# Kernel optimization log

Hardware: AMD Instinct MI355X
Metric: run time of the kernel (lower is better)

## Reference

```python
import jax, jax.numpy as jnp
import numpy as np

B, S, D, H, E, K, DH = 4, 1024, 1024, 8, 4, 2, 128


def setup_inputs() -> dict:
    key = jax.random.key(0)
    ks = jax.random.split(key, 9)
    std = 1.0 / np.sqrt(D)
    f = lambda k, shape, s: jax.random.normal(k, shape, dtype=jnp.float32) * s
    return {
        'q_src': f(ks[0], (B, S, D), 1.0),
        'k_src': f(ks[1], (B, S, D), 1.0),
        'v_src': f(ks[2], (B, S, D), 1.0),
        'Wq': f(ks[3], (H * DH, D), std),
        'Wk': f(ks[4], (H * DH, D), std),
        'Wv': f(ks[5], (H * E, D, DH), std),
        'Wo': f(ks[6], (H * E, DH, D), 1.0 / np.sqrt(H * DH)),
        'sel_v': f(ks[7], (H * E, D), std),
        'sel_o': f(ks[8], (H * E, D), std),
    }


def _route(src, selw):
    # sigmoid-gated per-head top-k expert selection (get_sel), eval mode
    g = jax.nn.sigmoid((src @ selw.T).reshape(*src.shape[:-1], H, E))  # [B,S,H,E]
    val, idx = jax.lax.top_k(g, K)
    # dense per-expert mixture weights: zeros except top-k sigmoid gates
    return (jax.nn.one_hot(idx, E, dtype=g.dtype) * val[..., None]).sum(-2)  # [B,S,H,E]


def reference(q_src, k_src, v_src, Wq, Wk, Wv, Wo, sel_v, sel_o):
    scale = (1.0 / np.sqrt(DH)) ** 0.5  # scale.sqrt() applied to both q and k
    q = ((q_src @ Wq.T) * scale).reshape(B, S, H, DH).transpose(0, 2, 1, 3)  # [B,H,S,DH]
    k = ((k_src @ Wk.T) * scale).reshape(B, S, H, DH).transpose(0, 2, 1, 3)

    wv = _route(k_src, sel_v)  # [B,S,H,E] V-expert gates (from keys)
    wo = _route(q_src, sel_o)  # [B,S,H,E] O-expert gates (from queries)

    # cvmm V: per-token top-k mixture of expert V projections
    v_all = jnp.einsum('bsd,hedc->bshec', v_src, Wv.reshape(H, E, D, DH))
    v = jnp.einsum('bshec,bshe->bhsc', v_all, wv)  # [B,H,S,DH]

    att = jax.nn.softmax(jnp.einsum('bhqc,bhkc->bhqk', q, k), axis=-1)
    res = jnp.einsum('bhqk,bhkc->bqhc', att, v)  # [B,S,H,DH]

    # cvmm O: weight per-head outputs by gates, project and sum over heads/experts
    resw = res[..., None, :] * wo[..., None]  # [B,S,H,E,DH]
    out = jnp.einsum('bshec,hecd->bsd', resw, Wo.reshape(H, E, DH, D))
    return out
```

## Files before the change

### kernel.cpp

```cpp
#include <hip/hip_runtime.h>

#define DEV __device__ __forceinline__

typedef __attribute__((ext_vector_type(8))) short s8v;
typedef __attribute__((ext_vector_type(4))) short s4v;
typedef __attribute__((ext_vector_type(4))) float f4v;

DEV unsigned short f2b(float f){
    unsigned u = __float_as_uint(f);
    u = (u + 0x7FFFu + ((u >> 16) & 1u)) >> 16;
    return (unsigned short)u;
}
DEV float b2f(short s){ return __uint_as_float(((unsigned)(unsigned short)s) << 16); }

DEV unsigned cvtpk(float lo, float hi){
    unsigned r;
    asm("v_cvt_pk_bf16_f32 %0, %1, %2" : "=v"(r) : "v"(lo), "v"(hi));
    return r;
}
DEV float exp2v(float x){
    float r;
    asm("v_exp_f32 %0, %1" : "=v"(r) : "v"(x));
    return r;
}

DEV void gload16(const void* g, void* l){
    __builtin_amdgcn_global_load_lds(
        (const __attribute__((address_space(1))) unsigned*)g,
        (__attribute__((address_space(3))) unsigned*)l, 16, 0, 0);
}


DEV void stage2(const short* A, const short* B, int sA, int sB, int kA, int kB,
                short* la, short* lb, int w, int lane){
    int srow = lane >> 3;
    int swcol = ((lane & 7) ^ srow) << 3;
    #pragma unroll
    for(int it = 0; it < 4; it++){
        int seg = (w << 2) + it;
        int row = (seg << 3) + srow;
        gload16(&A[(size_t)row * sA + kA + swcol], &la[seg << 9]);
        gload16(&B[(size_t)row * sB + kB + swcol], &lb[seg << 9]);
    }
}

DEV void mfma_block(const short* la, const short* lb, int wm, int wn, int qr, int grp, f4v acc[4][4]){
    #pragma unroll
    for(int ks = 0; ks < 2; ks++){
        s8v af[4], bf[4];
        #pragma unroll
        for(int m = 0; m < 4; m++)
            af[m] = *(const s8v*)&la[(wm + m * 16 + qr) * 64 + ((((ks << 2) + grp) ^ (qr & 7)) << 3)];
        #pragma unroll
        for(int n = 0; n < 4; n++)
            bf[n] = *(const s8v*)&lb[(wn + n * 16 + qr) * 64 + ((((ks << 2) + grp) ^ (qr & 7)) << 3)];
        #pragma unroll
        for(int m = 0; m < 4; m++)
            #pragma unroll
            for(int n = 0; n < 4; n++)
                acc[m][n] = __builtin_amdgcn_mfma_f32_16x16x32_bf16(af[m], bf[n], acc[m][n], 0, 0, 0);
    }
}

__global__ __launch_bounds__(256) void k_prep(const float* q_src, const float* k_src, const float* v_src,
                                              const float* Wq, const float* Wk, const float* Wv,
                                              const float* Wo, const float* selv, const float* selo,
                                              short* qsb, short* ksb, short* vsb, short* wqb, short* wkb,
                                              short* wvt, short* wot, float* part){
    __shared__ __align__(16) char smem[23040];
    int bid = blockIdx.x, tid = threadIdx.x;
    if(bid < 7168){
        int y, idx;
        if(bid < 6144){ y = bid >> 11; idx = (bid & 2047) * 256 + tid; }
        else { int i = bid - 6144; y = 3 + (i >> 9); idx = (i & 511) * 256 + tid; }
        const float* s = (y == 0) ? q_src : (y == 1) ? k_src : (y == 2) ? v_src : (y == 3) ? Wq : Wk;
        short* o = (y == 0) ? qsb : (y == 1) ? ksb : (y == 2) ? vsb : (y == 3) ? wqb : wkb;
        const float4* f = (const float4*)(s + (size_t)idx * 8);
        float4 a = f[0], b = f[1];
        s8v v;
        v[0] = f2b(a.x); v[1] = f2b(a.y); v[2] = f2b(a.z); v[3] = f2b(a.w);
        v[4] = f2b(b.x); v[5] = f2b(b.y); v[6] = f2b(b.z); v[7] = f2b(b.w);
        *(s8v*)(o + (size_t)idx * 8) = v;
    } else if(bid < 15360){
        const float* in; short* out; int R, C, c0, r0;
        if(bid < 11264){
            int i = bid - 7168;
            int z = i >> 7, rem = i & 127;
            R = 1024; C = 128;
            c0 = (rem & 3) * 32; r0 = (rem >> 2) * 32;
            in = Wv + (size_t)z * 131072;
            out = wvt + (size_t)z * 131072;
        } else {
            int i = bid - 11264;
            R = 4096; C = 1024;
            c0 = (i & 31) * 32; r0 = (i >> 5) * 32;
            in = Wo; out = wot;
        }
        float (*t)[33] = (float(*)[33])smem;
        int tx = tid & 31, ty = tid >> 5;
        #pragma unroll
        for(int p = 0; p < 4; p++){
            int r = p * 8 + ty;
            t[r][tx] = in[(size_t)(r0 + r) * C + c0 + tx];
        }
        __syncthreads();
        #pragma unroll
        for(int p = 0; p < 4; p++){
            int c = p * 8 + ty;
            out[(size_t)(c0 + c) * R + r0 + tx] = (short)f2b(t[tx][c]);
        }
    } else {
        int i = bid - 15360;
        int which = i & 1, bx = i >> 1;
        const float* src = which ? q_src : k_src;
        const float* sel = which ? selo : selv;
        int tt = bx >> 3, ks = bx & 7;
        int tok0 = tt << 7;
        float* lsrc = (float*)smem;
        float* lsel = (float*)(smem + 18432);
        int ts = tid & 31, es = tid >> 5;
        float acc[4][4];
        #pragma unroll
        for(int j = 0; j < 4; j++)
            #pragma unroll
            for(int q = 0; q < 4; q++) acc[j][q] = 0.f;
        #pragma unroll 1
        for(int c = 0; c < 4; c++){
            int k0 = (ks << 7) + (c << 5);
            {
                int row = tid >> 1, half = tid & 1;
                const float4* g = (const float4*)(src + (size_t)(tok0 + row) * 1024 + k0 + half * 16);
                #pragma unroll
                for(int qq = 0; qq < 4; qq++){
                    int qw = half * 4 + qq;
                    *(float4*)&lsrc[row * 36 + ((qw + row) & 7) * 4] = g[qq];
                }
            }
            {
                int row = tid >> 3, qw = tid & 7;
                *(float4*)&lsel[row * 36 + ((qw + row) & 7) * 4] =
                    *(const float4*)(sel + (size_t)row * 1024 + k0 + qw * 4);
            }
            __syncthreads();
            #pragma unroll
            for(int q = 0; q < 8; q++){
                float4 sv[4];
                #pragma unroll
                for(int v = 0; v < 4; v++){
                    int e = es * 4 + v;
                    sv[v] = *(const float4*)&lsel[e * 36 + ((q + e) & 7) * 4];
                }
                int slot = ((q + ts) & 7) * 4;
                #pragma unroll
                for(int j = 0; j < 4; j++){
                    float4 xv = *(const float4*)&lsrc[(ts + 32 * j) * 36 + slot];
                    #pragma unroll
                    for(int v = 0; v < 4; v++){
                        acc[j][v] = fmaf(xv.x, sv[v].x, acc[j][v]);
                        acc[j][v] = fmaf(xv.y, sv[v].y, acc[j][v]);
                        acc[j][v] = fmaf(xv.z, sv[v].z, acc[j][v]);
                        acc[j][v] = fmaf(xv.w, sv[v].w, acc[j][v]);
                    }
                }
            }
            __syncthreads();
        }
        #pragma unroll
        for(int j = 0; j < 4; j++){
            int token = tok0 + ts + 32 * j;
            f4v st;
            #pragma unroll
            for(int v = 0; v < 4; v++) st[v] = acc[j][v];
            *(f4v*)&part[(((size_t)(ks * 2 + which) * 4096) + token) * 32 + es * 4] = st;
        }
    }
}

__global__ __launch_bounds__(256) void k_rfinal(const float* part, float* wvp, float* wop){
    int which = blockIdx.y;
    float* wout = which ? wop : wvp;
    int tid = threadIdx.x;
    int tok = blockIdx.x * 32 + (tid >> 3), h = tid & 7;
    f4v sum = {0.f, 0.f, 0.f, 0.f};
    #pragma unroll
    for(int s = 0; s < 8; s++)
        sum += *(const f4v*)&part[(((size_t)(s * 2 + which) * 4096) + tok) * 32 + h * 4];
    float g[4];
    #pragma unroll
    for(int e = 0; e < 4; e++) g[e] = 1.0f / (1.0f + expf(-sum[e]));
    f4v out;
    #pragma unroll
    for(int e = 0; e < 4; e++){
        int rank = 0;
        #pragma unroll
        for(int j = 0; j < 4; j++)
            rank += (g[j] > g[e]) || (g[j] == g[e] && j < e);
        out[e] = (rank < 2) ? g[e] : 0.0f;
    }
    *(f4v*)&wout[(size_t)tok * 32 + h * 4] = out;
}

__global__ __launch_bounds__(256) void k_count(const float* wv, int* cntv){
    int he = blockIdx.x, tid = threadIdx.x;
    __shared__ int red[256];
    int c = 0;
    #pragma unroll
    for(int p = 0; p < 16; p++)
        c += (wv[(size_t)(p * 256 + tid) * 32 + he] > 0.f) ? 1 : 0;
    red[tid] = c;
    __syncthreads();
    for(int s = 128; s > 0; s >>= 1){
        if(tid < s) red[tid] += red[tid + s];
        __syncthreads();
    }
    if(tid == 0) cntv[he] = red[0];
}

__global__ __launch_bounds__(256) void k_scan(const int* cntv, int* basev, int* descv){
    __shared__ int ntl[33];
    int tid = threadIdx.x;
    if(tid == 0){
        int run = 0;
        for(int he = 0; he < 32; he++){
            ntl[he] = run;
            run += (cntv[he] + 127) >> 7;
        }
        ntl[32] = run;
    }
    __syncthreads();
    if(tid < 32) basev[tid] = ntl[tid] << 7;
    for(int i = tid; i < 544; i += 256){
        int d = -1;
        for(int he = 0; he < 32; he++)
            if(i >= ntl[he] && i < ntl[he + 1]) d = he;
        descv[i] = d;
    }
}

__global__ __launch_bounds__(256) void k_gather(const float* wv, const int* basev,
                                                int* idxv, float* gbufv, int* rpos){
    int he = blockIdx.x, h = he >> 2, e = he & 3;
    int tid = threadIdx.x, lane = tid & 63, w = tid >> 6;
    int base = basev[he];
    __shared__ int wsum[4];
    __shared__ int running;
    if(tid == 0) running = 0;
    __syncthreads();
    #pragma unroll 1
    for(int p = 0; p < 16; p++){
        int t = p * 256 + tid;
        float g = wv[(size_t)t * 32 + he];
        bool sel = g > 0.f;
        unsigned long long m = __ballot(sel);
        int lpref = __popcll(m & ((1ull << lane) - 1ull));
        if(lane == 0) wsum[w] = __popcll(m);
        __syncthreads();
        int rb = running;
        int woff = 0;
        #pragma unroll
        for(int j = 0; j < 4; j++) woff += (j < w) ? wsum[j] : 0;
        if(sel){
            int pos = base + rb + woff + lpref;
            idxv[pos] = t;
            gbufv[pos] = g;
            int slot = 0;
            #pragma unroll
            for(int j = 0; j < 4; j++)
                slot += (j < e && wv[(size_t)t * 32 + h * 4 + j] > 0.f) ? 1 : 0;
            rpos[(size_t)t * 16 + h * 2 + slot] = pos;
        }
        __syncthreads();
        if(tid == 0) running += wsum[0] + wsum[1] + wsum[2] + wsum[3];
        __syncthreads();
    }
    int tot = running;
    int aligned = (tot + 127) & ~127;
    for(int i = tid; i < aligned - tot; i += 256){
        idxv[base + tot + i] = 0;
        gbufv[base + tot + i] = 0.f;
    }
}

__global__ __launch_bounds__(256) void k_gemmqkg(const short* qsb, const short* ksb,
                                                 const short* wqb, const short* wkb,
                                                 short* qo, short* ko, float scale,
                                                 const short* vsb, const short* wvt,
                                                 const int* descv, const int* idxv,
                                                 const float* gbufv, short* Cg){
    __shared__ __align__(16) short la[2][8192];
    __shared__ __align__(16) short lb[2][8192];
    __shared__ int lidx[128];
    int bid = blockIdx.x;
    int tid = threadIdx.x, lane = tid & 63, w = tid >> 6;
    int wm = (w >> 1) << 6, wn = (w & 1) << 6;
    int qr = lane & 15, grp = lane >> 4;
    if(bid < 512){
        int wg = (bid & 7) * 64 + (bid >> 3);
        int which = wg >> 8, tl = wg & 255;
        int mt = tl >> 3, nt = tl & 7;
        const short* A = (which ? ksb : qsb) + ((size_t)(mt << 7)) * 1024;
        const short* B = (which ? wkb : wqb) + ((size_t)(nt << 7)) * 1024;
        short* out = which ? ko : qo;
        f4v acc[4][4];
        #pragma unroll
        for(int m = 0; m < 4; m++)
            #pragma unroll
            for(int n = 0; n < 4; n++) acc[m][n] = f4v{0.f, 0.f, 0.f, 0.f};
        #pragma unroll 1
        for(int t = -1; t < 16; t++){
            int nxt = t + 1;
            if(nxt < 16)
                stage2(A, B, 1024, 1024, nxt << 6, nxt << 6, la[nxt & 1], lb[nxt & 1], w, lane);
            if(t >= 0)
                mfma_block(la[t & 1], lb[t & 1], wm, wn, qr, grp, acc);
            __syncthreads();
        }
        #pragma unroll
        for(int m = 0; m < 4; m++){
            int rb = (mt << 7) + wm + m * 16 + (grp << 2);
            #pragma unroll
            for(int n = 0; n < 4; n++){
                int col = (nt << 7) + wn + n * 16 + qr;
                #pragma unroll
                for(int r = 0; r < 4; r++)
                    out[(size_t)(rb + r) * 1024 + col] = (short)f2b(acc[m][n][r] * scale);
            }
        }
    } else {
        int gb = bid - 512;
        int he = descv[gb];
        if(he < 0) return;
        int row0 = gb << 7;
        if(tid < 128) lidx[tid] = idxv[row0 + tid];
        __syncthreads();
        int srow = lane >> 3;
        int swcol = ((lane & 7) ^ srow) << 3;
        int arow[4];
        #pragma unroll
        for(int it = 0; it < 4; it++) arow[it] = lidx[(((w << 2) + it) << 3) + srow];
        const short* Bb = wvt + ((size_t)he << 17);
        f4v acc[4][4];
        #pragma unroll
        for(int m = 0; m < 4; m++)
            #pragma unroll
            for(int n = 0; n < 4; n++) acc[m][n] = f4v{0.f, 0.f, 0.f, 0.f};
        #pragma unroll 1
        for(int t = -1; t < 16; t++){
            int nxt = t + 1;
            if(nxt < 16){
                int buf = nxt & 1, k0 = nxt << 6;
                #pragma unroll
                for(int it = 0; it < 4; it++){
                    int seg = (w << 2) + it;
                    int row = (seg << 3) + srow;
                    gload16(&vsb[(size_t)arow[it] * 1024 + k0 + swcol], &la[buf][seg << 9]);
                    gload16(&Bb[(size_t)row * 1024 + k0 + swcol], &lb[buf][seg << 9]);
                }
            }
            if(t >= 0)
                mfma_block(la[t & 1], lb[t & 1], wm, wn, qr, grp, acc);
            __syncthreads();
        }
        #pragma unroll
        for(int m = 0; m < 4; m++){
            int rl = wm + m * 16 + (grp << 2);
            #pragma unroll
            for(int r = 0; r < 4; r++){
                float g = gbufv[row0 + rl + r];
                #pragma unroll
                for(int n = 0; n < 4; n++){
                    int col = wn + n * 16 + qr;
                    Cg[(size_t)(row0 + rl + r) * 128 + col] = (short)f2b(acc[m][n][r] * g);
                }
            }
        }
    }
}

__global__ __launch_bounds__(256) void k_vcomb(const short* Cg, const int* rpos, short* vtg){
    int bh = blockIdx.y, b = bh >> 3, h = bh & 7;
    int s0 = blockIdx.x * 32;
    __shared__ __align__(16) short t0[32][136];
    __shared__ __align__(16) short t1[32][136];
    __shared__ int rl[32][2];
    int tid = threadIdx.x;
    if(tid < 64){
        int i = tid >> 1, s = tid & 1;
        rl[i][s] = rpos[(size_t)(b * 1024 + s0 + i) * 16 + h * 2 + s];
    }
    __syncthreads();
    #pragma unroll
    for(int p = 0; p < 4; p++){
        int ch = tid + p * 256;
        int i = ch >> 5, slot = (ch >> 4) & 1, c8 = (ch & 15) << 3;
        s8v v = *(const s8v*)&Cg[(size_t)rl[i][slot] * 128 + c8];
        if(slot) *(s8v*)&t1[i][c8] = v;
        else     *(s8v*)&t0[i][c8] = v;
    }
    __syncthreads();
    #pragma unroll
    for(int p = 0; p < 16; p++){
        int idx = tid + p * 256;
        int s = idx & 31, c = idx >> 5;
        float v = b2f(t0[s][c]) + b2f(t1[s][c]);
        vtg[((size_t)bh * 128 + c) * 1024 + s0 + s] = (short)f2b(v);
    }
}

__global__ __launch_bounds__(256) void k_gemmo(const short* resw, const short* wot, float* po){
    __shared__ __align__(16) short la[2][8192];
    __shared__ __align__(16) short lb[2][8192];
    int wg = (blockIdx.x & 7) * 64 + (blockIdx.x >> 3);
    int ksp = wg & 1, tile = wg >> 1;
    int mt = tile >> 3, nt = tile & 7;
    const short* A = resw + (size_t)(mt << 7) * 4096 + ksp * 2048;
    const short* B = wot + (size_t)(nt << 7) * 4096 + ksp * 2048;
    int tid = threadIdx.x, lane = tid & 63, w = tid >> 6;
    int wm = (w >> 1) << 6, wn = (w & 1) << 6;
    int qr = lane & 15, grp = lane >> 4;
    f4v acc[4][4];
    #pragma unroll
    for(int m = 0; m < 4; m++)
        #pragma unroll
        for(int n = 0; n < 4; n++) acc[m][n] = f4v{0.f, 0.f, 0.f, 0.f};
    #pragma unroll 1
    for(int t = -1; t < 32; t++){
        int nxt = t + 1;
        if(nxt < 32)
            stage2(A, B, 4096, 4096, nxt << 6, nxt << 6, la[nxt & 1], lb[nxt & 1], w, lane);
        if(t >= 0)
            mfma_block(la[t & 1], lb[t & 1], wm, wn, qr, grp, acc);
        __syncthreads();
    }
    po += (size_t)ksp * 4194304;
    #pragma unroll
    for(int m = 0; m < 4; m++){
        int rb = (mt << 7) + wm + m * 16 + (grp << 2);
        #pragma unroll
        for(int n = 0; n < 4; n++){
            int col = (nt << 7) + wn + n * 16 + qr;
            #pragma unroll
            for(int r = 0; r < 4; r++)
                po[(size_t)(rb + r) * 1024 + col] = acc[m][n][r];
        }
    }
}

__global__ __launch_bounds__(256) void k_red(const float* p0, const float* p1, float* out){
    size_t idx = ((size_t)blockIdx.x * 256 + threadIdx.x) * 4;
    f4v a = *(const f4v*)&p0[idx];
    f4v b = *(const f4v*)&p1[idx];
    f4v s = a + b;
    *(f4v*)&out[idx] = s;
}

__global__ __launch_bounds__(256) void k_attn(const short* qg, const short* kg,
                                              const short* vtg, const float* wo, short* resw){
    __shared__ __align__(16) short lk[2][8192];
    __shared__ __align__(16) short lv[2][8192];
    __shared__ __align__(16) short pl[4][16 * 72];
    int swz = ((int)blockIdx.x & 7) * 64 + ((int)blockIdx.x >> 3);
    int bh = swz >> 4, qt = swz & 15;
    int b = bh >> 3, h = bh & 7;
    int w = threadIdx.x >> 6, lane = threadIdx.x & 63;
    int qr = lane & 15, grp = lane >> 4;
    int q0 = qt * 64 + w * 16;
    const short* vtb = vtg + ((size_t)bh << 17);
    short* pw = &pl[w][0];

    int tok = b * 1024 + q0 + qr;
    s8v qf[4];
    #pragma unroll
    for(int ks = 0; ks < 4; ks++)
        qf[ks] = *(const s8v*)&qg[(size_t)tok * 1024 + h * 128 + ks * 32 + grp * 8];
    f4v o[8];
    #pragma unroll
    for(int ct = 0; ct < 8; ct++) o[ct] = f4v{0.f, 0.f, 0.f, 0.f};
    float m_cur = -1e30f, l_lane = 0.f;

    int klr = lane >> 4, klc = lane & 15;
    int vlr = lane >> 3, vlc = lane & 7;

    #pragma unroll 1
    for(int t = -1; t < 16; t++){
        int nxt = t + 1;
        if(nxt < 16){
            int buf = nxt & 1, kv0 = nxt << 6;
            #pragma unroll
            for(int i = 0; i < 4; i++){
                int seg = (w << 2) + i;
                int kr = (seg << 2) + klr;
                int kc = klc ^ (kr & 7);
                gload16(&kg[(size_t)(b * 1024 + kv0 + kr) * 1024 + h * 128 + kc * 8], &lk[buf][seg << 9]);
                int vr = (seg << 3) + vlr;
                int vc = vlc ^ (vr & 7);
                gload16(&vtb[(size_t)vr * 1024 + kv0 + vc * 8], &lv[buf][seg << 9]);
            }
        }
        if(t >= 0){
            int cur = t & 1;
            f4v s[4];
            #pragma unroll
            for(int kt = 0; kt < 4; kt++) s[kt] = f4v{0.f, 0.f, 0.f, 0.f};
            __builtin_amdgcn_s_setprio(1);
            #pragma unroll
            for(int ks = 0; ks < 4; ks++){
                #pragma unroll
                for(int kt = 0; kt < 4; kt++){
                    int row = kt * 16 + qr;
                    s8v kf = *(const s8v*)&lk[cur][row * 128 + ((((ks << 2) + grp) ^ (row & 7)) << 3)];
                    s[kt] = __builtin_amdgcn_mfma_f32_16x16x32_bf16(kf, qf[ks], s[kt], 0, 0, 0);
                }
            }
            __builtin_amdgcn_s_setprio(0);
            float pm = s[0][0];
            #pragma unroll
            for(int kt = 0; kt < 4; kt++)
                #pragma unroll
                for(int r = 0; r < 4; r++) pm = fmaxf(pm, s[kt][r]);
            if(!__all(pm - m_cur <= 11.541f)){
                pm = fmaxf(pm, __shfl_xor(pm, 16));
                pm = fmaxf(pm, __shfl_xor(pm, 32));
                float mn = fmaxf(m_cur, pm);
                float fs = exp2v(m_cur - mn);
                #pragma unroll
                for(int ct = 0; ct < 8; ct++){
                    o[ct][0] *= fs; o[ct][1] *= fs; o[ct][2] *= fs; o[ct][3] *= fs;
                }
                l_lane *= fs;
                m_cur = mn;
            }
            #pragma unroll
            for(int kt = 0; kt < 4; kt++)
                #pragma unroll
                for(int r = 0; r < 4; r++){
                    s[kt][r] = exp2v(s[kt][r] - m_cur);
                    l_lane += s[kt][r];
                }
            #pragma unroll
            for(int kt = 0; kt < 4; kt++){
                uint2 pv;
                pv.x = cvtpk(s[kt][0], s[kt][1]);
                pv.y = cvtpk(s[kt][2], s[kt][3]);
                *(uint2*)&pw[qr * 72 + kt * 16 + grp * 4] = pv;
            }
            s8v pf0 = *(const s8v*)&pw[qr * 72 + grp * 8];
            s8v pf1 = *(const s8v*)&pw[qr * 72 + 32 + grp * 8];
            __builtin_amdgcn_s_setprio(1);
            #pragma unroll
            for(int ct = 0; ct < 8; ct++){
                int row = ct * 16 + qr;
                s8v vf0 = *(const s8v*)&lv[cur][row * 64 + ((grp ^ (row & 7)) << 3)];
                s8v vf1 = *(const s8v*)&lv[cur][row * 64 + (((4 + grp) ^ (row & 7)) << 3)];
                o[ct] = __builtin_amdgcn_mfma_f32_16x16x32_bf16(vf0, pf0, o[ct], 0, 0, 0);
                o[ct] = __builtin_amdgcn_mfma_f32_16x16x32_bf16(vf1, pf1, o[ct], 0, 0, 0);
            }
            __builtin_amdgcn_s_setprio(0);
        }
        __syncthreads();
    }
    l_lane += __shfl_xor(l_lane, 16);
    l_lane += __shfl_xor(l_lane, 32);
    float inv = 1.0f / l_lane;
    float g4[4];
    #pragma unroll
    for(int e = 0; e < 4; e++) g4[e] = wo[(size_t)tok * 32 + h * 4 + e];
    #pragma unroll
    for(int ct = 0; ct < 8; ct++){
        float v0 = o[ct][0] * inv, v1 = o[ct][1] * inv;
        float v2 = o[ct][2] * inv, v3 = o[ct][3] * inv;
        #pragma unroll
        for(int e = 0; e < 4; e++){
            uint2 sv;
            sv.x = cvtpk(v0 * g4[e], v1 * g4[e]);
            sv.y = cvtpk(v2 * g4[e], v3 * g4[e]);
            *(uint2*)&resw[(size_t)tok * 4096 + (h * 4 + e) * 128 + ct * 16 + grp * 4] = sv;
        }
    }
}

extern "C" void kernel_launch(void* const* d_in, const int* in_sizes, int n_in,
                              void* d_out, int out_size, void* d_ws, size_t ws_size,
                              hipStream_t stream){
    const float* q_src = (const float*)d_in[0];
    const float* k_src = (const float*)d_in[1];
    const float* v_src = (const float*)d_in[2];
    const float* Wq    = (const float*)d_in[3];
    const float* Wk    = (const float*)d_in[4];
    const float* Wv    = (const float*)d_in[5];
    const float* Wo    = (const float*)d_in[6];
    const float* selv  = (const float*)d_in[7];
    const float* selo  = (const float*)d_in[8];

    const size_t MB = 1ull << 20;
    char* ws = (char*)d_ws;
    short* qsb  = (short*)(ws + 0 * MB);
    short* ksb  = (short*)(ws + 8 * MB);
    short* vsb  = (short*)(ws + 16 * MB);
    short* wqb  = (short*)(ws + 24 * MB);
    short* wkb  = (short*)(ws + 26 * MB);
    short* wvt  = (short*)(ws + 28 * MB);
    short* wot  = (short*)(ws + 36 * MB);
    short* q    = (short*)(ws + 44 * MB);
    short* k    = (short*)(ws + 52 * MB);
    short* vt   = (short*)(ws + 60 * MB);
    float* wv   = (float*)(ws + 76 * MB);
    float* wo   = (float*)(ws + 76 * MB + 524288);
    float* part = (float*)(ws + 80 * MB);
    short* Cg   = (short*)(ws + 80 * MB);
    int*   cntv = (int*)  (ws + 100 * MB);
    int*   basev= (int*)  (ws + 100 * MB + 4096);
    int*   descv= (int*)  (ws + 100 * MB + 8192);
    int*   idxv = (int*)  (ws + 101 * MB);
    float* gbufv= (float*)(ws + 102 * MB);
    int*   rposv= (int*)  (ws + 103 * MB);
    short* resw = (short*)(ws + 0 * MB);
    float* po   = (float*)(ws + 80 * MB);

    const float qk_scale = 0.29730177875068026f * 1.2011224087864498f;

    k_prep<<<dim3(15872), 256, 0, stream>>>(q_src, k_src, v_src, Wq, Wk, Wv, Wo, selv, selo,
                                            qsb, ksb, vsb, wqb, wkb, wvt, wot, part);
    k_rfinal<<<dim3(128, 2), 256, 0, stream>>>(part, wv, wo);
    k_count<<<dim3(32), 256, 0, stream>>>(wv, cntv);
    k_scan<<<dim3(1), 256, 0, stream>>>(cntv, basev, descv);
    k_gather<<<dim3(32), 256, 0, stream>>>(wv, basev, idxv, gbufv, rposv);
    k_gemmqkg<<<dim3(1056), 256, 0, stream>>>(qsb, ksb, wqb, wkb, q, k, qk_scale,
                                              vsb, wvt, descv, idxv, gbufv, Cg);
    k_vcomb<<<dim3(32, 32), 256, 0, stream>>>(Cg, rposv, vt);
    k_attn<<<dim3(512), 256, 0, stream>>>(q, k, vt, wo, resw);
    k_gemmo<<<dim3(512), 256, 0, stream>>>(resw, wot, po);
    k_red<<<dim3(4096), 256, 0, stream>>>(po, po + 4194304, (float*)d_out);
}
```

Before: 219.4 us.

## Fuse routing count and scan into neighbors; single-buffer QK/V gather GEMM

Expert counts are now accumulated in k_rfinal through shared and global atomics, and the prefix scan plus descriptor fill moves into k_gather. This drops two small kernel launches (k_count, k_scan), at the cost of one memset. Separately, the QK and gathered-V GEMM drops LDS double buffering for a single buffer with two barriers per K step. That halves LDS use, which may raise occupancy, but it removes the overlap between global loads and MFMA.

```diff
diff --git a/kernel.cpp b/kernel.cpp
--- a/kernel.cpp
+++ b/kernel.cpp
@@ -176,10 +176,13 @@
     }
 }
 
-__global__ __launch_bounds__(256) void k_rfinal(const float* part, float* wvp, float* wop){
+__global__ __launch_bounds__(256) void k_rfinal(const float* part, float* wvp, float* wop, int* cntv){
     int which = blockIdx.y;
     float* wout = which ? wop : wvp;
+    __shared__ int cnt[32];
     int tid = threadIdx.x;
+    if(tid < 32) cnt[tid] = 0;
+    __syncthreads();
     int tok = blockIdx.x * 32 + (tid >> 3), h = tid & 7;
     f4v sum = {0.f, 0.f, 0.f, 0.f};
     #pragma unroll
@@ -196,52 +199,29 @@
         for(int j = 0; j < 4; j++)
             rank += (g[j] > g[e]) || (g[j] == g[e] && j < e);
         out[e] = (rank < 2) ? g[e] : 0.0f;
+        if(which == 0 && out[e] > 0.f) atomicAdd(&cnt[h * 4 + e], 1);
     }
     *(f4v*)&wout[(size_t)tok * 32 + h * 4] = out;
-}
-
-__global__ __launch_bounds__(256) void k_count(const float* wv, int* cntv){
-    int he = blockIdx.x, tid = threadIdx.x;
-    __shared__ int red[256];
-    int c = 0;
-    #pragma unroll
-    for(int p = 0; p < 16; p++)
-        c += (wv[(size_t)(p * 256 + tid) * 32 + he] > 0.f) ? 1 : 0;
-    red[tid] = c;
     __syncthreads();
-    for(int s = 128; s > 0; s >>= 1){
-        if(tid < s) red[tid] += red[tid + s];
-        __syncthreads();
-    }
-    if(tid == 0) cntv[he] = red[0];
-}
-
-__global__ __launch_bounds__(256) void k_scan(const int* cntv, int* basev, int* descv){
+    if(which == 0 && tid < 32 && cnt[tid]) atomicAdd(&cntv[tid], cnt[tid]);
+}
+
+__global__ __launch_bounds__(256) void k_gather(const float* wv, const int* cntv,
+                                                int* idxv, float* gbufv, int* rpos, int* descv){
+    int he = blockIdx.x, h = he >> 2, e = he & 3;
+    int tid = threadIdx.x, lane = tid & 63, w = tid >> 6;
     __shared__ int ntl[33];
-    int tid = threadIdx.x;
     if(tid == 0){
         int run = 0;
-        for(int he = 0; he < 32; he++){
-            ntl[he] = run;
-            run += (cntv[he] + 127) >> 7;
-        }
+        #pragma unroll
+        for(int j = 0; j < 32; j++){ ntl[j] = run; run += (cntv[j] + 127) >> 7; }
         ntl[32] = run;
     }
     __syncthreads();
-    if(tid < 32) basev[tid] = ntl[tid] << 7;
-    for(int i = tid; i < 544; i += 256){
-        int d = -1;
-        for(int he = 0; he < 32; he++)
-            if(i >= ntl[he] && i < ntl[he + 1]) d = he;
-        descv[i] = d;
-    }
-}
-
-__global__ __launch_bounds__(256) void k_gather(const float* wv, const int* basev,
-                                                int* idxv, float* gbufv, int* rpos){
-    int he = blockIdx.x, h = he >> 2, e = he & 3;
-    int tid = threadIdx.x, lane = tid & 63, w = tid >> 6;
-    int base = basev[he];
+    int base = ntl[he] << 7;
+    for(int i = ntl[he] + tid; i < ntl[he + 1]; i += 256) descv[i] = he;
+    if(he == 0)
+        for(int i = ntl[32] + tid; i < 544; i += 256) descv[i] = -1;
     __shared__ int wsum[4];
     __shared__ int running;
     if(tid == 0) running = 0;
@@ -287,8 +267,8 @@
                                                  const short* vsb, const short* wvt,
                                                  const int* descv, const int* idxv,
                                                  const float* gbufv, short* Cg){
-    __shared__ __align__(16) short la[2][8192];
-    __shared__ __align__(16) short lb[2][8192];
+    __shared__ __align__(16) short la[8192];
+    __shared__ __align__(16) short lb[8192];
     __shared__ int lidx[128];
     int bid = blockIdx.x;
     int tid = threadIdx.x, lane = tid & 63, w = tid >> 6;
@@ -307,12 +287,10 @@
             #pragma unroll
             for(int n = 0; n < 4; n++) acc[m][n] = f4v{0.f, 0.f, 0.f, 0.f};
         #pragma unroll 1
-        for(int t = -1; t < 16; t++){
-            int nxt = t + 1;
-            if(nxt < 16)
-                stage2(A, B, 1024, 1024, nxt << 6, nxt << 6, la[nxt & 1], lb[nxt & 1], w, lane);
-            if(t >= 0)
-                mfma_block(la[t & 1], lb[t & 1], wm, wn, qr, grp, acc);
+        for(int t = 0; t < 16; t++){
+            stage2(A, B, 1024, 1024, t << 6, t << 6, la, lb, w, lane);
+            __syncthreads();
+            mfma_block(la, lb, wm, wn, qr, grp, acc);
             __syncthreads();
         }
         #pragma unroll
@@ -345,20 +323,17 @@
             #pragma unroll
             for(int n = 0; n < 4; n++) acc[m][n] = f4v{0.f, 0.f, 0.f, 0.f};
         #pragma unroll 1
-        for(int t = -1; t < 16; t++){
-            int nxt = t + 1;
-            if(nxt < 16){
-                int buf = nxt & 1, k0 = nxt << 6;
-                #pragma unroll
-                for(int it = 0; it < 4; it++){
-                    int seg = (w << 2) + it;
-                    int row = (seg << 3) + srow;
-                    gload16(&vsb[(size_t)arow[it] * 1024 + k0 + swcol], &la[buf][seg << 9]);
-                    gload16(&Bb[(size_t)row * 1024 + k0 + swcol], &lb[buf][seg << 9]);
-                }
-            }
-            if(t >= 0)
-                mfma_block(la[t & 1], lb[t & 1], wm, wn, qr, grp, acc);
+        for(int t = 0; t < 16; t++){
+            int k0 = t << 6;
+            #pragma unroll
+            for(int it = 0; it < 4; it++){
+                int seg = (w << 2) + it;
+                int row = (seg << 3) + srow;
+                gload16(&vsb[(size_t)arow[it] * 1024 + k0 + swcol], &la[seg << 9]);
+                gload16(&Bb[(size_t)row * 1024 + k0 + swcol], &lb[seg << 9]);
+            }
+            __syncthreads();
+            mfma_block(la, lb, wm, wn, qr, grp, acc);
             __syncthreads();
         }
         #pragma unroll
@@ -609,7 +584,6 @@
     float* part = (float*)(ws + 80 * MB);
     short* Cg   = (short*)(ws + 80 * MB);
     int*   cntv = (int*)  (ws + 100 * MB);
-    int*   basev= (int*)  (ws + 100 * MB + 4096);
     int*   descv= (int*)  (ws + 100 * MB + 8192);
     int*   idxv = (int*)  (ws + 101 * MB);
     float* gbufv= (float*)(ws + 102 * MB);
@@ -619,12 +593,11 @@
 
     const float qk_scale = 0.29730177875068026f * 1.2011224087864498f;
 
+    hipMemsetAsync(cntv, 0, 128, stream);
     k_prep<<<dim3(15872), 256, 0, stream>>>(q_src, k_src, v_src, Wq, Wk, Wv, Wo, selv, selo,
                                             qsb, ksb, vsb, wqb, wkb, wvt, wot, part);
-    k_rfinal<<<dim3(128, 2), 256, 0, stream>>>(part, wv, wo);
-    k_count<<<dim3(32), 256, 0, stream>>>(wv, cntv);
-    k_scan<<<dim3(1), 256, 0, stream>>>(cntv, basev, descv);
-    k_gather<<<dim3(32), 256, 0, stream>>>(wv, basev, idxv, gbufv, rposv);
+    k_rfinal<<<dim3(128, 2), 256, 0, stream>>>(part, wv, wo, cntv);
+    k_gather<<<dim3(32), 256, 0, stream>>>(wv, cntv, idxv, gbufv, rposv, descv);
     k_gemmqkg<<<dim3(1056), 256, 0, stream>>>(qsb, ksb, wqb, wkb, q, k, qk_scale,
                                               vsb, wvt, descv, idxv, gbufv, Cg);
     k_vcomb<<<dim3(32, 32), 256, 0, stream>>>(Cg, rposv, vt);
```

Measured after the change: 225.1 us. +2.6%, slower.
